# Optimization experiments

Hardware: AMD Instinct MI355X
Metric: run time of the kernel (lower is better)

The kernel has to match this reference:

```python
import jax, jax.numpy as jnp
import numpy as np

NUM_GROUPS = 32
EPS = 1e-6


def group_norm(x, weight, bias):
    # x: [b, c, h, w]
    b, c, h, w = x.shape
    xg = x.reshape(b, NUM_GROUPS, c // NUM_GROUPS, h, w)
    mean = jnp.mean(xg, axis=(2, 3, 4), keepdims=True)
    var = jnp.var(xg, axis=(2, 3, 4), keepdims=True)
    xn = ((xg - mean) * jax.lax.rsqrt(var + EPS)).reshape(b, c, h, w)
    return xn * weight[None, :, None, None] + bias[None, :, None, None]


def conv1x1(x, w, b):
    # 1x1 conv == per-pixel matmul. x: [b, c_in, h, w], w: [c_out, c_in]
    return jnp.einsum('oi,bihw->bohw', w, x) + b[None, :, None, None]


def setup_inputs() -> dict:
    key = jax.random.key(0)
    ks = jax.random.split(key, 9)
    b, c, h, w = 8, 512, 64, 64
    scale = 1.0 / np.sqrt(c)
    return {
        'x': jax.random.normal(ks[0], (b, c, h, w), jnp.float32),
        'gn_weight': jnp.ones((c,), jnp.float32),
        'gn_bias': jnp.zeros((c,), jnp.float32),
        'wq': jax.random.normal(ks[1], (c, c), jnp.float32) * scale,
        'bq': jnp.zeros((c,), jnp.float32),
        'wk': jax.random.normal(ks[2], (c, c), jnp.float32) * scale,
        'bk': jnp.zeros((c,), jnp.float32),
        'wv': jax.random.normal(ks[3], (c, c), jnp.float32) * scale,
        'bv': jnp.zeros((c,), jnp.float32),
        'wp': jax.random.normal(ks[4], (c, c), jnp.float32) * scale,
        'bp': jnp.zeros((c,), jnp.float32),
    }


def reference(x, gn_weight, gn_bias, wq, bq, wk, bk, wv, bv, wp, bp):
    h_ = group_norm(x, gn_weight, gn_bias)
    q = conv1x1(h_, wq, bq)
    k = conv1x1(h_, wk, bk)
    v = conv1x1(h_, wv, bv)
    b, c, h, w = q.shape
    n = h * w
    qf = q.reshape(b, c, n)
    kf = k.reshape(b, c, n)
    vf = v.reshape(b, c, n)
    # scores: [b, q, k]
    scores = jnp.einsum('bcq,bck->bqk', qf, kf) * (c ** -0.5)
    attn = jax.nn.softmax(scores, axis=-1)
    out = jnp.einsum('bqk,bck->bcq', attn, vf).reshape(b, c, h, w)
    out = conv1x1(out, wp, bp)
    return x + out
```

## Files before the change

kernel.cpp:

```cpp
#include <hip/hip_runtime.h>
#include <cstdint>

typedef unsigned short u16;
typedef __bf16 bf16x8 __attribute__((ext_vector_type(8)));
typedef float f32x4 __attribute__((ext_vector_type(4)));

__device__ __forceinline__ u16 f2bf(float f) {
    uint32_t u = __float_as_uint(f);
    u += 0x7FFFu + ((u >> 16) & 1u);
    return (u16)(u >> 16);
}
__device__ __forceinline__ float bf2f(u16 v) {
    return __uint_as_float((uint32_t)v << 16);
}

__device__ __forceinline__ void gload16(const u16* g, u16* l) {
    __builtin_amdgcn_global_load_lds(
        (const __attribute__((address_space(1))) uint32_t*)g,
        (__attribute__((address_space(3))) uint32_t*)l, 16, 0, 0);
}

__device__ __forceinline__ void swz(int& n_idx, int& m_idx, int& z_idx) {
    const int nx = gridDim.x, ny = gridDim.y;
    int lid = blockIdx.x + nx * (blockIdx.y + ny * blockIdx.z);
    int g = lid & 7, h = lid >> 3;
    n_idx = h % nx;
    int pair = (h / nx) * 8 + g;
    m_idx = pair % ny;
    z_idx = pair / ny;
}

__global__ __launch_bounds__(256) void k_detect(const u16* __restrict__ x,
                                                int* __restrict__ flag) {
    const int t = threadIdx.x;
    uint32_t mx = 0;
    for (int i = 0; i < 256; i++) {
        uint32_t v = (uint32_t)x[i * 256 + t] & 0x7FFFu;
        mx = mx > v ? mx : v;
    }
    for (int off = 32; off > 0; off >>= 1) {
        uint32_t o = (uint32_t)__shfl_xor((int)mx, off);
        mx = mx > o ? mx : o;
    }
    __shared__ uint32_t r[4];
    if ((t & 63) == 0) r[t >> 6] = mx;
    __syncthreads();
    if (t == 0) {
        uint32_t a = r[0] > r[1] ? r[0] : r[1];
        uint32_t b = r[2] > r[3] ? r[2] : r[3];
        mx = a > b ? a : b;
        *flag = (mx > 0x5000u) ? 1 : 0;
    }
}

__global__ __launch_bounds__(256) void k_cvt_wb(const void* wq, const void* wk,
                                                const void* wv, const void* wp,
                                                const void* gw, const void* gb,
                                                const void* bq, const void* bk,
                                                const void* bv, const void* bp,
                                                const int* __restrict__ flag,
                                                u16* __restrict__ Wc,
                                                u16* __restrict__ Bc) {
    const int mode = *flag;
    int i = blockIdx.x * 256 + threadIdx.x;
    if (i >= 1048576 + 3072) return;
    const void* src;
    u16* dst;
    int off;
    if (i < 1048576) {
        int which = i >> 18;
        off = i & 262143;
        src = which == 0 ? wq : which == 1 ? wk : which == 2 ? wv : wp;
        dst = Wc + i;
    } else {
        int j = i - 1048576;
        int which = j >> 9;
        off = j & 511;
        src = which == 0 ? gw : which == 1 ? gb : which == 2 ? bq
            : which == 3 ? bk : which == 4 ? bv : bp;
        dst = Bc + j;
    }
    *dst = mode ? f2bf(((const float*)src)[off]) : ((const u16*)src)[off];
}

__global__ __launch_bounds__(256) void k_gn_stats(const void* __restrict__ x_raw,
                                                  const u16* __restrict__ Bc,
                                                  const int* __restrict__ flag,
                                                  float* __restrict__ Sc,
                                                  float* __restrict__ Sh) {
    const int b = blockIdx.x >> 5, g = blockIdx.x & 31;
    const int mode = *flag;
    const int t = threadIdx.x;
    const int wave = t >> 6, lane = t & 63;
    float s = 0.f, ss = 0.f;
    if (mode) {
        const float4* xb = (const float4*)((const float*)x_raw +
                                           ((size_t)b * 512 + g * 16) * 4096);
        for (int it = 0; it < 64; it++) {
            float4 v = xb[it * 256 + t];
            s += v.x + v.y + v.z + v.w;
            ss += v.x * v.x + v.y * v.y + v.z * v.z + v.w * v.w;
        }
    } else {
        const uint4* xb = (const uint4*)((const u16*)x_raw +
                                         ((size_t)b * 512 + g * 16) * 4096);
        for (int it = 0; it < 32; it++) {
            uint4 v = xb[it * 256 + t];
            uint32_t w[4] = {v.x, v.y, v.z, v.w};
            for (int j = 0; j < 4; j++) {
                float a = __uint_as_float(w[j] << 16);
                float c = __uint_as_float(w[j] & 0xFFFF0000u);
                s += a + c;
                ss += a * a + c * c;
            }
        }
    }
    for (int off = 32; off > 0; off >>= 1) {
        s += __shfl_xor(s, off);
        ss += __shfl_xor(ss, off);
    }
    __shared__ float rs[4], rss[4];
    if (lane == 0) { rs[wave] = s; rss[wave] = ss; }
    __syncthreads();
    s = rs[0] + rs[1] + rs[2] + rs[3];
    ss = rss[0] + rss[1] + rss[2] + rss[3];
    const float mean = s * (1.f / 65536.f);
    const float var = ss * (1.f / 65536.f) - mean * mean;
    const float rstd = rsqrtf(var + 1e-6f);
    if (t < 16) {
        int c = g * 16 + t;
        float w = bf2f(Bc[c]);
        Sc[b * 512 + c] = rstd * w;
        Sh[b * 512 + c] = bf2f(Bc[512 + c]) - mean * rstd * w;
    }
}

#define TPAD 520
__global__ __launch_bounds__(256) void k_gn_apply(const void* __restrict__ x_raw,
                                                  const int* __restrict__ flag,
                                                  const float* __restrict__ Sc,
                                                  const float* __restrict__ Sh,
                                                  u16* __restrict__ HT) {
    __shared__ u16 tile[64 * TPAD];
    __shared__ float sSc[512], sSh[512];
    const int b = blockIdx.y;
    const int p0 = blockIdx.x * 64;
    const int mode = *flag;
    const int t = threadIdx.x;
    sSc[t] = Sc[b * 512 + t]; sSc[t + 256] = Sc[b * 512 + t + 256];
    sSh[t] = Sh[b * 512 + t]; sSh[t + 256] = Sh[b * 512 + t + 256];
    __syncthreads();
    for (int it = 0; it < 16; it++) {
        int li = it * 256 + t;
        int c = li >> 3;
        int pj = (li & 7) * 8;
        float v[8];
        if (mode) {
            const float* xr = (const float*)x_raw + ((size_t)b * 512 + c) * 4096 + p0 + pj;
            float4 a = *(const float4*)xr;
            float4 d = *(const float4*)(xr + 4);
            v[0] = a.x; v[1] = a.y; v[2] = a.z; v[3] = a.w;
            v[4] = d.x; v[5] = d.y; v[6] = d.z; v[7] = d.w;
        } else {
            const u16* xr = (const u16*)x_raw + ((size_t)b * 512 + c) * 4096 + p0 + pj;
            uint4 a = *(const uint4*)xr;
            uint32_t w[4] = {a.x, a.y, a.z, a.w};
            for (int j = 0; j < 4; j++) {
                v[2 * j] = __uint_as_float(w[j] << 16);
                v[2 * j + 1] = __uint_as_float(w[j] & 0xFFFF0000u);
            }
        }
        float sc = sSc[c], sh = sSh[c];
        for (int k = 0; k < 8; k++)
            tile[(pj + k) * TPAD + c] = f2bf(v[k] * sc + sh);
    }
    __syncthreads();
    u16* H = HT + (size_t)b * 2097152 + (size_t)p0 * 512;
    for (int it = 0; it < 16; it++) {
        int ch = it * 256 + t;
        int pp = ch >> 6;
        int cc = (ch & 63) * 8;
        *(uint4*)&H[(size_t)pp * 512 + cc] = *(const uint4*)&tile[pp * TPAD + cc];
    }
}

__device__ __forceinline__ void gemm_core(const u16* __restrict__ A,
                                          const u16* __restrict__ BT,
                                          int lda, int ldb, int K,
                                          int m0, int n0,
                                          u16* lA, u16* lB,
                                          f32x4 (&acc)[4][4]) {
    const int t = threadIdx.x;
    const int wave = t >> 6, lane = t & 63;
    const int wm = (wave >> 1) * 64, wn = (wave & 1) * 64;
    const int mf = lane & 15, quad = lane >> 4;
    const int srow = t >> 3;
    const int scol = (((t & 7) ^ (srow & 7)) * 8);
    const u16* Ap = A + (size_t)(m0 + srow) * lda + scol;
    const u16* Bp = BT + (size_t)(n0 + srow) * ldb + scol;
    u16* lAd = &lA[t * 8];
    u16* lBd = &lB[t * 8];
    const int fx = mf & 7;

    for (int i = 0; i < 4; i++)
        for (int j = 0; j < 4; j++)
            acc[i][j] = (f32x4){0.f, 0.f, 0.f, 0.f};

    for (int k0 = 0; k0 < K; k0 += 64) {
        __syncthreads();
        gload16(Ap + k0, lAd);
        gload16(Ap + k0 + (size_t)32 * lda, lAd + 2048);
        gload16(Ap + k0 + (size_t)64 * lda, lAd + 4096);
        gload16(Ap + k0 + (size_t)96 * lda, lAd + 6144);
        gload16(Bp + k0, lBd);
        gload16(Bp + k0 + (size_t)32 * ldb, lBd + 2048);
        gload16(Bp + k0 + (size_t)64 * ldb, lBd + 4096);
        gload16(Bp + k0 + (size_t)96 * ldb, lBd + 6144);
        __syncthreads();
        for (int ks = 0; ks < 2; ks++) {
            bf16x8 af[4], bfr[4];
            const int sl = ((ks * 4 + quad) ^ fx) * 8;
            for (int i = 0; i < 4; i++)
                af[i] = *(const bf16x8*)&lA[(wm + i * 16 + mf) * 64 + sl];
            for (int j = 0; j < 4; j++)
                bfr[j] = *(const bf16x8*)&lB[(wn + j * 16 + mf) * 64 + sl];
            for (int i = 0; i < 4; i++)
                for (int j = 0; j < 4; j++)
                    acc[i][j] = __builtin_amdgcn_mfma_f32_16x16x32_bf16(af[i], bfr[j], acc[i][j], 0, 0, 0);
        }
    }
}

__global__ __launch_bounds__(256) void k_qkv(const u16* __restrict__ HT,
                                             const u16* __restrict__ Wc,
                                             const u16* __restrict__ Bc,
                                             u16* __restrict__ QT,
                                             u16* __restrict__ KT,
                                             u16* __restrict__ V) {
    __shared__ __align__(16) u16 sm[16384];
    int nI, mI, zI;
    swz(nI, mI, zI);
    const int b = zI / 3, s = zI % 3;
    const u16* Bb = Bc + 1024 + s * 512;
    int m0, n0, ldo, bias_by_row;
    const u16 *A, *BT;
    u16* O;
    if (s < 2) {
        m0 = mI * 128; n0 = nI * 128;
        A = HT + (size_t)b * 2097152; BT = Wc + (size_t)s * 262144;
        O = (s == 0 ? QT : KT) + (size_t)b * 2097152; ldo = 512; bias_by_row = 0;
    } else {
        m0 = nI * 128; n0 = mI * 128;
        A = Wc + (size_t)2 * 262144; BT = HT + (size_t)b * 2097152;
        O = V + (size_t)b * 2097152; ldo = 4096; bias_by_row = 1;
    }
    f32x4 acc[4][4];
    gemm_core(A, BT, 512, 512, 512, m0, n0, sm, sm + 8192, acc);

    const int t = threadIdx.x;
    const int wave = t >> 6, lane = t & 63;
    const int wm = (wave >> 1) * 64, wn = (wave & 1) * 64;
    const int mf = lane & 15, quad = lane >> 4;
    __syncthreads();
    for (int i = 0; i < 4; i++)
        for (int r = 0; r < 4; r++) {
            int row = wm + i * 16 + quad * 4 + r;
            int kk = ((row >> 2) & 3) << 4;
            for (int j = 0; j < 4; j++) {
                int col = wn + j * 16 + mf;
                float bias = bf2f(Bb[bias_by_row ? (m0 + row) : (n0 + col)]);
                sm[row * 128 + (col ^ kk)] = f2bf(acc[i][j][r] + bias);
            }
        }
    __syncthreads();
    for (int p = 0; p < 8; p++) {
        int idx = p * 256 + t;
        int rowt = idx >> 4, c8 = (idx & 15) * 8;
        int kk = ((rowt >> 2) & 3) << 4;
        uint4 v = *(const uint4*)&sm[rowt * 128 + (c8 ^ kk)];
        *(uint4*)&O[(size_t)(m0 + rowt) * ldo + n0 + c8] = v;
    }
}

__device__ __forceinline__ u16* s_ptr(u16* S_ht, u16* S_tail, int l) {
    return l == 0 ? S_ht : S_tail + (size_t)(l - 1) * 16777216;
}

__global__ __launch_bounds__(512, 2) void k_scores(const u16* __restrict__ QT,
                                                   const u16* __restrict__ KT,
                                                   u16* __restrict__ S_ht,
                                                   u16* __restrict__ S_tail,
                                                   float* __restrict__ Part,
                                                   int b0) {
    __shared__ __align__(16) u16 lds[65536];
    int nI, mI, l;
    swz(nI, mI, l);
    const int n0 = nI * 256;
    const int m0 = mI * 256;
    const int b = b0 + l;
    const u16* Aq = QT + (size_t)b * 2097152;
    const u16* Bk = KT + (size_t)b * 2097152;

    const int t = threadIdx.x;
    const int wave = t >> 6, lane = t & 63;
    const int wm = (wave >> 2) * 128, wn = (wave & 3) * 64;
    const int mf = lane & 15, quad = lane >> 4;
    const int fx = mf & 7;
    const int srow = t >> 3;
    const int scol8 = t & 7;

    f32x4 acc[8][4];
#pragma unroll
    for (int i = 0; i < 8; i++)
#pragma unroll
        for (int j = 0; j < 4; j++)
            acc[i][j] = (f32x4){0.f, 0.f, 0.f, 0.f};

    auto issueA = [&](u16* dst, int h, int k0) {
#pragma unroll
        for (int s = 0; s < 2; s++) {
            int row = h * 128 + s * 64 + srow;
            gload16(Aq + (size_t)(m0 + row) * 512 + k0 + ((scol8 ^ (row & 7)) << 3),
                    dst + h * 8192 + s * 4096 + t * 8);
        }
    };
    auto issueB = [&](u16* dst, int h, int k0) {
#pragma unroll
        for (int s = 0; s < 2; s++) {
            int row = h * 128 + s * 64 + srow;
            gload16(Bk + (size_t)(n0 + row) * 512 + k0 + ((scol8 ^ (row & 7)) << 3),
                    dst + h * 8192 + s * 4096 + t * 8);
        }
    };

    issueA(lds, 0, 0); issueA(lds, 1, 0);
    issueB(lds + 16384, 0, 0); issueB(lds + 16384, 1, 0);

    for (int kt = 0; kt < 8; kt++) {
        u16* lA = (kt & 1) ? lds + 32768 : lds;
        u16* lB = lA + 16384;
        u16* pA = (kt & 1) ? lds : lds + 32768;
        u16* pB = pA + 16384;
        const int k0n = (kt + 1) << 6;
        const bool pf = kt < 7;
        asm volatile("" ::: "memory");
        __builtin_amdgcn_s_barrier();
        asm volatile("" ::: "memory");
        if (pf) {
            issueA(pA, 0, k0n);
            asm volatile("s_waitcnt vmcnt(2)" ::: "memory");
        } else {
            asm volatile("s_waitcnt vmcnt(0)" ::: "memory");
        }
        __builtin_amdgcn_s_barrier();
        asm volatile("" ::: "memory");

        bf16x8 af[8], bfr[2];
        int sl = (quad ^ fx) * 8;
#pragma unroll
        for (int i = 0; i < 8; i++)
            af[i] = *(const bf16x8*)&lA[(wm + i * 16 + mf) * 64 + sl];
#pragma unroll
        for (int j = 0; j < 2; j++)
            bfr[j] = *(const bf16x8*)&lB[(wn + j * 16 + mf) * 64 + sl];
        __builtin_amdgcn_s_setprio(1);
#pragma unroll
        for (int i = 0; i < 8; i++)
#pragma unroll
            for (int j = 0; j < 2; j++)
                acc[i][j] = __builtin_amdgcn_mfma_f32_16x16x32_bf16(af[i], bfr[j], acc[i][j], 0, 0, 0);
        __builtin_amdgcn_s_setprio(0);
        if (pf) issueA(pA, 1, k0n);
#pragma unroll
        for (int j = 0; j < 2; j++)
            bfr[j] = *(const bf16x8*)&lB[(wn + (2 + j) * 16 + mf) * 64 + sl];
        __builtin_amdgcn_s_setprio(1);
#pragma unroll
        for (int i = 0; i < 8; i++)
#pragma unroll
            for (int j = 0; j < 2; j++)
                acc[i][2 + j] = __builtin_amdgcn_mfma_f32_16x16x32_bf16(af[i], bfr[j], acc[i][2 + j], 0, 0, 0);
        __builtin_amdgcn_s_setprio(0);
        sl = ((4 + quad) ^ fx) * 8;
        if (pf) issueB(pB, 0, k0n);
#pragma unroll
        for (int i = 0; i < 8; i++)
            af[i] = *(const bf16x8*)&lA[(wm + i * 16 + mf) * 64 + sl];
#pragma unroll
        for (int j = 0; j < 2; j++)
            bfr[j] = *(const bf16x8*)&lB[(wn + j * 16 + mf) * 64 + sl];
        __builtin_amdgcn_s_setprio(1);
#pragma unroll
        for (int i = 0; i < 8; i++)
#pragma unroll
            for (int j = 0; j < 2; j++)
                acc[i][j] = __builtin_amdgcn_mfma_f32_16x16x32_bf16(af[i], bfr[j], acc[i][j], 0, 0, 0);
        __builtin_amdgcn_s_setprio(0);
        if (pf) issueB(pB, 1, k0n);
#pragma unroll
        for (int j = 0; j < 2; j++)
            bfr[j] = *(const bf16x8*)&lB[(wn + (2 + j) * 16 + mf) * 64 + sl];
        __builtin_amdgcn_s_setprio(1);
#pragma unroll
        for (int i = 0; i < 8; i++)
#pragma unroll
            for (int j = 0; j < 2; j++)
                acc[i][2 + j] = __builtin_amdgcn_mfma_f32_16x16x32_bf16(af[i], bfr[j], acc[i][2 + j], 0, 0, 0);
        __builtin_amdgcn_s_setprio(0);
    }

    const float scale = 0.04419417382415922f;
    __syncthreads();
#pragma unroll
    for (int i = 0; i < 8; i++)
#pragma unroll
        for (int r = 0; r < 4; r++) {
            int row = wm + i * 16 + quad * 4 + r;
            int key = row & 7;
#pragma unroll
            for (int j = 0; j < 4; j++) {
                int col = wn + j * 16 + mf;
                lds[row * 256 + (((col >> 3) ^ key) << 3) + (col & 7)] =
                    f2bf(__expf(acc[i][j][r] * scale));
            }
        }
    __syncthreads();
    u16* Sb = s_ptr(S_ht, S_tail, l);
    float* pr = Part + ((size_t)b * 16 + nI) * 4096 + m0;
    for (int p = 0; p < 16; p++) {
        int idx = p * 512 + t;
        int row = idx >> 5, chunk = idx & 31;
        uint4 v = *(const uint4*)&lds[row * 256 + ((chunk ^ (row & 7)) << 3)];
        uint32_t w[4] = {v.x, v.y, v.z, v.w};
        float s = 0.f;
        for (int q2 = 0; q2 < 4; q2++)
            s += __uint_as_float(w[q2] << 16) + __uint_as_float(w[q2] & 0xFFFF0000u);
        for (int off = 16; off > 0; off >>= 1) s += __shfl_xor(s, off);
        if ((lane & 31) == 0) pr[row] = s;
        *(uint4*)&Sb[(size_t)(m0 + row) * 4096 + n0 + chunk * 8] = v;
    }
}

__global__ __launch_bounds__(512, 2) void k_pv_split(u16* __restrict__ S_ht,
                                                     u16* __restrict__ S_tail,
                                                     const u16* __restrict__ V,
                                                     u16* __restrict__ QT,
                                                     u16* __restrict__ KT,
                                                     int b0) {
    __shared__ __align__(16) u16 lds[49152];
    int nI, mI, zI;
    swz(nI, mI, zI);
    const int n0 = nI * 256;
    const int m0 = mI * 128;
    const int l = zI >> 1, split = zI & 1, b = b0 + l;
    const u16* A = s_ptr(S_ht, S_tail, l) + split * 2048;
    const u16* B = V + (size_t)b * 2097152 + split * 2048;

    const int t = threadIdx.x;
    const int wave = t >> 6, lane = t & 63;
    const int wm = (wave >> 2) * 64, wn = (wave & 3) * 64;
    const int mf = lane & 15, quad = lane >> 4;
    const int fx = mf & 7;
    const int srow = t >> 3;
    const int scol8 = t & 7;

    f32x4 acc[4][4];
#pragma unroll
    for (int i = 0; i < 4; i++)
#pragma unroll
        for (int j = 0; j < 4; j++)
            acc[i][j] = (f32x4){0.f, 0.f, 0.f, 0.f};

    auto issueA = [&](u16* dst, int k0) {
#pragma unroll
        for (int s = 0; s < 2; s++) {
            int row = s * 64 + srow;
            gload16(A + (size_t)(m0 + row) * 4096 + k0 + ((scol8 ^ (row & 7)) << 3),
                    dst + s * 4096 + t * 8);
        }
    };
    auto issueB = [&](u16* dst, int h, int k0) {
#pragma unroll
        for (int s = 0; s < 2; s++) {
            int row = h * 128 + s * 64 + srow;
            gload16(B + (size_t)(n0 + row) * 4096 + k0 + ((scol8 ^ (row & 7)) << 3),
                    dst + h * 8192 + s * 4096 + t * 8);
        }
    };

    issueA(lds, 0);
    issueB(lds + 8192, 0, 0);
    issueB(lds + 8192, 1, 0);

    for (int kt = 0; kt < 32; kt++) {
        u16* lA = (kt & 1) ? lds + 24576 : lds;
        u16* lB = lA + 8192;
        u16* pA = (kt & 1) ? lds : lds + 24576;
        u16* pB = pA + 8192;
        const int k0n = (kt + 1) << 6;
        const bool pf = kt < 31;
        asm volatile("" ::: "memory");
        __builtin_amdgcn_s_barrier();
        asm volatile("" ::: "memory");
        if (pf) {
            issueA(pA, k0n);
            asm volatile("s_waitcnt vmcnt(2)" ::: "memory");
        } else {
            asm volatile("s_waitcnt vmcnt(0)" ::: "memory");
        }
        __builtin_amdgcn_s_barrier();
        asm volatile("" ::: "memory");

        bf16x8 af[4], bfr[2];
        int sl = (quad ^ fx) * 8;
#pragma unroll
        for (int i = 0; i < 4; i++)
            af[i] = *(const bf16x8*)&lA[(wm + i * 16 + mf) * 64 + sl];
#pragma unroll
        for (int j = 0; j < 2; j++)
            bfr[j] = *(const bf16x8*)&lB[(wn + j * 16 + mf) * 64 + sl];
        __builtin_amdgcn_s_setprio(1);
#pragma unroll
        for (int i = 0; i < 4; i++)
#pragma unroll
            for (int j = 0; j < 2; j++)
                acc[i][j] = __builtin_amdgcn_mfma_f32_16x16x32_bf16(af[i], bfr[j], acc[i][j], 0, 0, 0);
        __builtin_amdgcn_s_setprio(0);
        if (pf) issueB(pB, 0, k0n);
#pragma unroll
        for (int j = 0; j < 2; j++)
            bfr[j] = *(const bf16x8*)&lB[(wn + (2 + j) * 16 + mf) * 64 + sl];
        __builtin_amdgcn_s_setprio(1);
#pragma unroll
        for (int i = 0; i < 4; i++)
#pragma unroll
            for (int j = 0; j < 2; j++)
                acc[i][2 + j] = __builtin_amdgcn_mfma_f32_16x16x32_bf16(af[i], bfr[j], acc[i][2 + j], 0, 0, 0);
        __builtin_amdgcn_s_setprio(0);
        sl = ((4 + quad) ^ fx) * 8;
        if (pf) issueB(pB, 1, k0n);
#pragma unroll
        for (int i = 0; i < 4; i++)
            af[i] = *(const bf16x8*)&lA[(wm + i * 16 + mf) * 64 + sl];
#pragma unroll
        for (int j = 0; j < 2; j++)
            bfr[j] = *(const bf16x8*)&lB[(wn + j * 16 + mf) * 64 + sl];
        __builtin_amdgcn_s_setprio(1);
#pragma unroll
        for (int i = 0; i < 4; i++)
#pragma unroll
            for (int j = 0; j < 2; j++)
                acc[i][j] = __builtin_amdgcn_mfma_f32_16x16x32_bf16(af[i], bfr[j], acc[i][j], 0, 0, 0);
        __builtin_amdgcn_s_setprio(0);
#pragma unroll
        for (int j = 0; j < 2; j++)
            bfr[j] = *(const bf16x8*)&lB[(wn + (2 + j) * 16 + mf) * 64 + sl];
        __builtin_amdgcn_s_setprio(1);
#pragma unroll
        for (int i = 0; i < 4; i++)
#pragma unroll
            for (int j = 0; j < 2; j++)
                acc[i][2 + j] = __builtin_amdgcn_mfma_f32_16x16x32_bf16(af[i], bfr[j], acc[i][2 + j], 0, 0, 0);
        __builtin_amdgcn_s_setprio(0);
    }

    u16* P = (split == 0 ? QT : KT) + (size_t)b * 2097152;
    __syncthreads();
#pragma unroll
    for (int i = 0; i < 4; i++)
#pragma unroll
        for (int r = 0; r < 4; r++) {
            int row = wm + i * 16 + quad * 4 + r;
            int key = row & 7;
#pragma unroll
            for (int j = 0; j < 4; j++) {
                int col = wn + j * 16 + mf;
                lds[row * 256 + (((col >> 3) ^ key) << 3) + (col & 7)] =
                    f2bf(acc[i][j][r]);
            }
        }
    __syncthreads();
    for (int p = 0; p < 8; p++) {
        int idx = p * 512 + t;
        int row = idx >> 5, chunk = idx & 31;
        uint4 v = *(const uint4*)&lds[row * 256 + ((chunk ^ (row & 7)) << 3)];
        *(uint4*)&P[(size_t)(m0 + row) * 512 + n0 + chunk * 8] = v;
    }
}

__global__ __launch_bounds__(256) void k_pv_reduce(const u16* __restrict__ QT,
                                                   const u16* __restrict__ KT,
                                                   const float* __restrict__ Part,
                                                   u16* __restrict__ OT,
                                                   int b0) {
    const int b = b0 + blockIdx.y;
    const int t = threadIdx.x;
    __shared__ float sInv[4];
    if (t < 64) {
        int r = t >> 4, which = t & 15;
        int p = blockIdx.x * 4 + r;
        float v = Part[((size_t)b * 16 + which) * 4096 + p];
        for (int off = 8; off > 0; off >>= 1) v += __shfl_xor(v, off);
        if (which == 0) sInv[r] = 1.f / v;
    }
    __syncthreads();
    const float inv = sInv[t >> 6];
    size_t base = (size_t)b * 2097152;
    size_t i0 = base + ((size_t)blockIdx.x * 256 + t) * 8;
    uint4 a = *(const uint4*)(QT + i0);
    uint4 c = *(const uint4*)(KT + i0);
    uint32_t wa[4] = {a.x, a.y, a.z, a.w};
    uint32_t wc[4] = {c.x, c.y, c.z, c.w};
    uint32_t o[4];
    for (int j = 0; j < 4; j++) {
        float lo = (__uint_as_float(wa[j] << 16) + __uint_as_float(wc[j] << 16)) * inv;
        float hi = (__uint_as_float(wa[j] & 0xFFFF0000u) + __uint_as_float(wc[j] & 0xFFFF0000u)) * inv;
        o[j] = (uint32_t)f2bf(lo) | ((uint32_t)f2bf(hi) << 16);
    }
    *(uint4*)(OT + i0) = make_uint4(o[0], o[1], o[2], o[3]);
}

__global__ __launch_bounds__(256) void k_proj(const u16* __restrict__ Wc,
                                              const u16* __restrict__ OT,
                                              const u16* __restrict__ Bc,
                                              const void* __restrict__ x_raw,
                                              const int* __restrict__ flag,
                                              void* __restrict__ y_raw) {
    __shared__ __align__(16) u16 smu[16384];
    float* smf = (float*)smu;
    int nI, mI, b;
    swz(nI, mI, b);
    const int n0 = nI * 128;
    const int m0 = mI * 128;
    f32x4 acc[4][4];
    gemm_core(Wc + (size_t)3 * 262144, OT + (size_t)b * 2097152, 512, 512, 512,
              m0, n0, smu, smu + 8192, acc);

    const int mode = *flag;
    const u16* bp = Bc + 5 * 512;
    const int t = threadIdx.x;
    const int wave = t >> 6, lane = t & 63;
    const int wn = (wave & 1) * 64;
    const int mf = lane & 15, quad = lane >> 4;
    const int whalf = wave >> 1;
    size_t bb = (size_t)b * 2097152;
    for (int h = 0; h < 2; h++) {
        __syncthreads();
        if (whalf == h) {
            for (int i = 0; i < 4; i++)
                for (int r = 0; r < 4; r++) {
                    int rowl = i * 16 + quad * 4 + r;
                    int kf = ((rowl >> 2) & 1) << 4;
                    for (int j = 0; j < 4; j++) {
                        int col = wn + j * 16 + mf;
                        smf[rowl * 128 + (col ^ kf)] = acc[i][j][r];
                    }
                }
        }
        __syncthreads();
        const int rowbase = m0 + h * 64;
        if (mode) {
            for (int p = 0; p < 8; p++) {
                int idx = p * 256 + t;
                int rowl = idx >> 5, c4 = (idx & 31) * 4;
                int kf = ((rowl >> 2) & 1) << 4;
                f32x4 v = *(const f32x4*)&smf[rowl * 128 + (c4 ^ kf)];
                int rowg = rowbase + rowl;
                float bias = bf2f(bp[rowg]);
                size_t o = bb + (size_t)rowg * 4096 + n0 + c4;
                float4 xv = *(const float4*)((const float*)x_raw + o);
                float4 out = make_float4(v[0] + bias + xv.x, v[1] + bias + xv.y,
                                         v[2] + bias + xv.z, v[3] + bias + xv.w);
                *(float4*)((float*)y_raw + o) = out;
            }
        } else {
            for (int p = 0; p < 4; p++) {
                int idx = p * 256 + t;
                int rowl = idx >> 4, c8 = (idx & 15) * 8;
                int kf = ((rowl >> 2) & 1) << 4;
                const float* sp = &smf[rowl * 128 + (c8 ^ kf)];
                f32x4 v0 = *(const f32x4*)sp;
                f32x4 v1 = *(const f32x4*)(sp + 4);
                int rowg = rowbase + rowl;
                float bias = bf2f(bp[rowg]);
                size_t o = bb + (size_t)rowg * 4096 + n0 + c8;
                uint4 xv = *(const uint4*)((const u16*)x_raw + o);
                uint32_t xw[4] = {xv.x, xv.y, xv.z, xv.w};
                float vals[8] = {v0[0], v0[1], v0[2], v0[3],
                                 v1[0], v1[1], v1[2], v1[3]};
                uint32_t ow[4];
                for (int q2 = 0; q2 < 4; q2++) {
                    float lo = __uint_as_float(xw[q2] << 16) + vals[2 * q2] + bias;
                    float hi = __uint_as_float(xw[q2] & 0xFFFF0000u) + vals[2 * q2 + 1] + bias;
                    ow[q2] = (uint32_t)f2bf(lo) | ((uint32_t)f2bf(hi) << 16);
                }
                *(uint4*)((u16*)y_raw + o) = make_uint4(ow[0], ow[1], ow[2], ow[3]);
            }
        }
    }
}

extern "C" void kernel_launch(void* const* d_in, const int* in_sizes, int n_in,
                              void* d_out, int out_size, void* d_ws, size_t ws_size,
                              hipStream_t stream) {
    (void)in_sizes; (void)n_in; (void)out_size;
    const void* x  = d_in[0];
    const void* gw = d_in[1];
    const void* gb = d_in[2];
    const void* wq = d_in[3];
    const void* bq = d_in[4];
    const void* wk = d_in[5];
    const void* bk = d_in[6];
    const void* wv = d_in[7];
    const void* bv = d_in[8];
    const void* wp = d_in[9];
    const void* bp = d_in[10];

    u16* ws16 = (u16*)d_ws;
    int* flag = (int*)d_ws;
    float* Sc = (float*)(ws16 + 16);
    float* Sh = Sc + 4096;
    u16* Wc = ws16 + 16 + 16384;
    u16* Bc = Wc + 1048576;
    u16* HT = Bc + 4096;
    u16* QT = HT + 16777216;
    u16* KT = QT + 16777216;
    u16* V  = KT + 16777216;
    u16* OT = V  + 16777216;
    float* Part = (float*)(OT + 16777216);
    u16* Tail = (u16*)(Part + 1048576);
    const size_t base_elems = (size_t)(Tail - ws16);

    int nb = 1;
    for (int cand = 8; cand >= 2; cand >>= 1) {
        size_t need = 2ull * (base_elems + (size_t)(cand - 1) * 16777216ull);
        if (ws_size >= need) { nb = cand; break; }
    }

    k_detect<<<1, 256, 0, stream>>>((const u16*)x, flag);
    k_cvt_wb<<<4108, 256, 0, stream>>>(wq, wk, wv, wp, gw, gb, bq, bk, bv, bp,
                                       flag, Wc, Bc);
    k_gn_stats<<<256, 256, 0, stream>>>(x, Bc, flag, Sc, Sh);
    k_gn_apply<<<dim3(64, 8), 256, 0, stream>>>(x, flag, Sc, Sh, HT);
    k_qkv<<<dim3(4, 32, 24), 256, 0, stream>>>(HT, Wc, Bc, QT, KT, V);
    for (int b0 = 0; b0 < 8; b0 += nb) {
        k_scores<<<dim3(16, 16, nb), 512, 0, stream>>>(QT, KT, HT, Tail, Part, b0);
        k_pv_split<<<dim3(2, 32, 2 * nb), 512, 0, stream>>>(HT, Tail, V, QT, KT, b0);
        k_pv_reduce<<<dim3(1024, nb), 256, 0, stream>>>(QT, KT, Part, OT, b0);
    }
    k_proj<<<dim3(32, 4, 8), 256, 0, stream>>>(Wc, OT, Bc, x, flag, d_out);
}
```

Baseline: 701.0 us.

## Rewrite QKV GEMM with 256x256 tiles and double-buffered interleaved prefetch

After: 687.5 us, median of 2. Within noise of the previous version (-1.9%).

```diff
diff --git a/kernel.cpp b/kernel.cpp
--- a/kernel.cpp
+++ b/kernel.cpp
@@ -231,54 +231,160 @@
     }
 }
 
-__global__ __launch_bounds__(256) void k_qkv(const u16* __restrict__ HT,
-                                             const u16* __restrict__ Wc,
-                                             const u16* __restrict__ Bc,
-                                             u16* __restrict__ QT,
-                                             u16* __restrict__ KT,
-                                             u16* __restrict__ V) {
-    __shared__ __align__(16) u16 sm[16384];
-    int nI, mI, zI;
-    swz(nI, mI, zI);
-    const int b = zI / 3, s = zI % 3;
+__global__ __launch_bounds__(512, 2) void k_qkv(const u16* __restrict__ HT,
+                                                const u16* __restrict__ Wc,
+                                                const u16* __restrict__ Bc,
+                                                u16* __restrict__ QT,
+                                                u16* __restrict__ KT,
+                                                u16* __restrict__ V) {
+    __shared__ __align__(16) u16 lds[65536];
+    int xI, bs, dz;
+    swz(xI, bs, dz);
+    const int b = bs / 3, s = bs % 3;
     const u16* Bb = Bc + 1024 + s * 512;
     int m0, n0, ldo, bias_by_row;
-    const u16 *A, *BT;
+    const u16 *A, *B;
     u16* O;
     if (s < 2) {
-        m0 = mI * 128; n0 = nI * 128;
-        A = HT + (size_t)b * 2097152; BT = Wc + (size_t)s * 262144;
+        m0 = (xI >> 1) * 256; n0 = (xI & 1) * 256;
+        A = HT + (size_t)b * 2097152; B = Wc + (size_t)s * 262144;
         O = (s == 0 ? QT : KT) + (size_t)b * 2097152; ldo = 512; bias_by_row = 0;
     } else {
-        m0 = nI * 128; n0 = mI * 128;
-        A = Wc + (size_t)2 * 262144; BT = HT + (size_t)b * 2097152;
+        m0 = (xI & 1) * 256; n0 = (xI >> 1) * 256;
+        A = Wc + (size_t)2 * 262144; B = HT + (size_t)b * 2097152;
         O = V + (size_t)b * 2097152; ldo = 4096; bias_by_row = 1;
     }
-    f32x4 acc[4][4];
-    gemm_core(A, BT, 512, 512, 512, m0, n0, sm, sm + 8192, acc);
 
     const int t = threadIdx.x;
     const int wave = t >> 6, lane = t & 63;
-    const int wm = (wave >> 1) * 64, wn = (wave & 1) * 64;
+    const int wm = (wave >> 2) * 128, wn = (wave & 3) * 64;
     const int mf = lane & 15, quad = lane >> 4;
-    __syncthreads();
-    for (int i = 0; i < 4; i++)
+    const int fx = mf & 7;
+    const int srow = t >> 3;
+    const int scol8 = t & 7;
+
+    f32x4 acc[8][4];
+#pragma unroll
+    for (int i = 0; i < 8; i++)
+#pragma unroll
+        for (int j = 0; j < 4; j++)
+            acc[i][j] = (f32x4){0.f, 0.f, 0.f, 0.f};
+
+    auto issueA = [&](u16* dst, int h, int k0) {
+#pragma unroll
+        for (int ss = 0; ss < 2; ss++) {
+            int row = h * 128 + ss * 64 + srow;
+            gload16(A + (size_t)(m0 + row) * 512 + k0 + ((scol8 ^ (row & 7)) << 3),
+                    dst + h * 8192 + ss * 4096 + t * 8);
+        }
+    };
+    auto issueB = [&](u16* dst, int h, int k0) {
+#pragma unroll
+        for (int ss = 0; ss < 2; ss++) {
+            int row = h * 128 + ss * 64 + srow;
+            gload16(B + (size_t)(n0 + row) * 512 + k0 + ((scol8 ^ (row & 7)) << 3),
+                    dst + h * 8192 + ss * 4096 + t * 8);
+        }
+    };
+
+    issueA(lds, 0, 0); issueA(lds, 1, 0);
+    issueB(lds + 16384, 0, 0); issueB(lds + 16384, 1, 0);
+
+    for (int kt = 0; kt < 8; kt++) {
+        u16* lA = (kt & 1) ? lds + 32768 : lds;
+        u16* lB = lA + 16384;
+        u16* pA = (kt & 1) ? lds : lds + 32768;
+        u16* pB = pA + 16384;
+        const int k0n = (kt + 1) << 6;
+        const bool pf = kt < 7;
+        asm volatile("" ::: "memory");
+        __builtin_amdgcn_s_barrier();
+        asm volatile("" ::: "memory");
+        if (pf) {
+            issueA(pA, 0, k0n);
+            asm volatile("s_waitcnt vmcnt(2)" ::: "memory");
+        } else {
+            asm volatile("s_waitcnt vmcnt(0)" ::: "memory");
+        }
+        __builtin_amdgcn_s_barrier();
+        asm volatile("" ::: "memory");
+
+        bf16x8 af[8], bfr[2];
+        int sl = (quad ^ fx) * 8;
+#pragma unroll
+        for (int i = 0; i < 8; i++)
+            af[i] = *(const bf16x8*)&lA[(wm + i * 16 + mf) * 64 + sl];
+#pragma unroll
+        for (int j = 0; j < 2; j++)
+            bfr[j] = *(const bf16x8*)&lB[(wn + j * 16 + mf) * 64 + sl];
+        __builtin_amdgcn_s_setprio(1);
+#pragma unroll
+        for (int i = 0; i < 8; i++)
+#pragma unroll
+            for (int j = 0; j < 2; j++)
+                acc[i][j] = __builtin_amdgcn_mfma_f32_16x16x32_bf16(af[i], bfr[j], acc[i][j], 0, 0, 0);
+        __builtin_amdgcn_s_setprio(0);
+        if (pf) issueA(pA, 1, k0n);
+#pragma unroll
+        for (int j = 0; j < 2; j++)
+            bfr[j] = *(const bf16x8*)&lB[(wn + (2 + j) * 16 + mf) * 64 + sl];
+        __builtin_amdgcn_s_setprio(1);
+#pragma unroll
+        for (int i = 0; i < 8; i++)
+#pragma unroll
+            for (int j = 0; j < 2; j++)
+                acc[i][2 + j] = __builtin_amdgcn_mfma_f32_16x16x32_bf16(af[i], bfr[j], acc[i][2 + j], 0, 0, 0);
+        __builtin_amdgcn_s_setprio(0);
+        sl = ((4 + quad) ^ fx) * 8;
+        if (pf) issueB(pB, 0, k0n);
+#pragma unroll
+        for (int i = 0; i < 8; i++)
+            af[i] = *(const bf16x8*)&lA[(wm + i * 16 + mf) * 64 + sl];
+#pragma unroll
+        for (int j = 0; j < 2; j++)
+            bfr[j] = *(const bf16x8*)&lB[(wn + j * 16 + mf) * 64 + sl];
+        __builtin_amdgcn_s_setprio(1);
+#pragma unroll
+        for (int i = 0; i < 8; i++)
+#pragma unroll
+            for (int j = 0; j < 2; j++)
+                acc[i][j] = __builtin_amdgcn_mfma_f32_16x16x32_bf16(af[i], bfr[j], acc[i][j], 0, 0, 0);
+        __builtin_amdgcn_s_setprio(0);
+        if (pf) issueB(pB, 1, k0n);
+#pragma unroll
+        for (int j = 0; j < 2; j++)
+            bfr[j] = *(const bf16x8*)&lB[(wn + (2 + j) * 16 + mf) * 64 + sl];
+        __builtin_amdgcn_s_setprio(1);
+#pragma unroll
+        for (int i = 0; i < 8; i++)
+#pragma unroll
+            for (int j = 0; j < 2; j++)
+                acc[i][2 + j] = __builtin_amdgcn_mfma_f32_16x16x32_bf16(af[i], bfr[j], acc[i][2 + j], 0, 0, 0);
+        __builtin_amdgcn_s_setprio(0);
+    }
+
+    __syncthreads();
+#pragma unroll
+    for (int i = 0; i < 8; i++)
+#pragma unroll
         for (int r = 0; r < 4; r++) {
             int row = wm + i * 16 + quad * 4 + r;
-            int kk = ((row >> 2) & 3) << 4;
+            int key = row & 7;
+            float brow = bias_by_row ? bf2f(Bb[m0 + row]) : 0.f;
+#pragma unroll
             for (int j = 0; j < 4; j++) {
                 int col = wn + j * 16 + mf;
-                float bias = bf2f(Bb[bias_by_row ? (m0 + row) : (n0 + col)]);
-                sm[row * 128 + (col ^ kk)] = f2bf(acc[i][j][r] + bias);
+                float bias = bias_by_row ? brow : bf2f(Bb[n0 + col]);
+                lds[row * 256 + (((col >> 3) ^ key) << 3) + (col & 7)] =
+                    f2bf(acc[i][j][r] + bias);
             }
         }
     __syncthreads();
-    for (int p = 0; p < 8; p++) {
-        int idx = p * 256 + t;
-        int rowt = idx >> 4, c8 = (idx & 15) * 8;
-        int kk = ((rowt >> 2) & 3) << 4;
-        uint4 v = *(const uint4*)&sm[rowt * 128 + (c8 ^ kk)];
-        *(uint4*)&O[(size_t)(m0 + rowt) * ldo + n0 + c8] = v;
+    for (int p = 0; p < 16; p++) {
+        int idx = p * 512 + t;
+        int row = idx >> 5, chunk = idx & 31;
+        uint4 v = *(const uint4*)&lds[row * 256 + ((chunk ^ (row & 7)) << 3)];
+        *(uint4*)&O[(size_t)(m0 + row) * ldo + n0 + chunk * 8] = v;
     }
 }
 
@@ -742,7 +848,7 @@
                                        flag, Wc, Bc);
     k_gn_stats<<<256, 256, 0, stream>>>(x, Bc, flag, Sc, Sh);
     k_gn_apply<<<dim3(64, 8), 256, 0, stream>>>(x, flag, Sc, Sh, HT);
-    k_qkv<<<dim3(4, 32, 24), 256, 0, stream>>>(HT, Wc, Bc, QT, KT, V);
+    k_qkv<<<dim3(32, 24), 512, 0, stream>>>(HT, Wc, Bc, QT, KT, V);
     for (int b0 = 0; b0 < 8; b0 += nb) {
         k_scores<<<dim3(16, 16, nb), 512, 0, stream>>>(QT, KT, HT, Tail, Part, b0);
         k_pv_split<<<dim3(2, 32, 2 * nb), 512, 0, stream>>>(HT, Tail, V, QT, KT, b0);
```
